# Kernel tuning notes

Hardware: AMD Instinct MI355X
Metric: run time of the kernel (lower is better)

The kernel has to match this reference:

```python
import jax, jax.numpy as jnp
import numpy as np

B, S, DIN, DOUT = 4, 2048, 4096, 4096
QMAX = 127  # 2**(8-1) - 1


def setup_inputs() -> dict:
    key = jax.random.key(0)
    k_x, k_w, k_b, k_ws = jax.random.split(key, 4)
    x = jax.random.normal(k_x, (B, S, DIN), dtype=jnp.float32)
    # int8-valued weights stored as int32 (as in the torch module's .int() weight)
    weight = jax.random.randint(k_w, (DOUT, DIN), -QMAX, QMAX + 1, dtype=jnp.int32)
    bias = jax.random.randint(k_b, (DOUT,), -10, 11, dtype=jnp.int32)
    # per-input-channel weight scale, shape (out_features, 1)
    weight_scale = (jax.random.uniform(k_ws, (DOUT, 1), dtype=jnp.float32) * 0.01 + 1e-4)
    input_scale = jnp.float32(0.02)
    output_scale = jnp.float32(0.05)
    return {
        "x": x,
        "weight": weight,
        "bias": bias,
        "weight_scale": weight_scale,
        "input_scale": input_scale,
        "output_scale": output_scale,
    }


def reference(x, weight, bias, weight_scale, input_scale, output_scale):
    # fake-quantize activations: round to int grid, then dequantize back to float
    xq = jnp.round(x / input_scale).astype(jnp.int32).astype(jnp.float32) * input_scale
    # dequantize weights: (O, I)
    w = weight.astype(jnp.float32) * weight_scale
    # fp32 GEMM: [B,S,I] x [I,O] -> [B,S,O]
    ret = jnp.einsum("bsi,oi->bso", xq, w)
    ret = ret + bias.astype(jnp.float32)
    # requantize output to int grid (int32 output, as in torch .int())
    return jnp.round(ret / output_scale).astype(jnp.int32)
```

## Files before the change

kernel.cpp:

```cpp
#include <hip/hip_runtime.h>
#include <stdint.h>

#define MDIM 8192
#define KDIM 4096
#define NDIM 4096
#define BK   64
#define NKT  (KDIM / BK)

typedef float f32x4 __attribute__((ext_vector_type(4)));
typedef __bf16 bf16x8 __attribute__((ext_vector_type(8)));
typedef short short8 __attribute__((ext_vector_type(8)));
typedef float fl4 __attribute__((ext_vector_type(4)));
typedef int i32x4 __attribute__((ext_vector_type(4)));

__device__ __forceinline__ short f2bf_bits(float f) {
    unsigned int u = __float_as_uint(f);
    u += 0x7fffu + ((u >> 16) & 1u);
    return (short)(u >> 16);
}

__device__ __forceinline__ void gload_lds16(const void* g, void* l) {
    __builtin_amdgcn_global_load_lds(
        (__attribute__((address_space(1))) void*)(uintptr_t)g,
        (__attribute__((address_space(3))) void*)(uintptr_t)l,
        16, 0, 0);
}

__global__ void __launch_bounds__(256) quant_x_kernel(const float* __restrict__ x,
                                                      short* __restrict__ xq,
                                                      const float* __restrict__ p_is) {
    const float inv_is = 1.0f / p_is[0];
    const int64_t stride = (int64_t)gridDim.x * 256 * 8;
    for (int64_t i = ((int64_t)blockIdx.x * 256 + threadIdx.x) * 8;
         i < (int64_t)MDIM * KDIM; i += stride) {
        fl4 a = __builtin_nontemporal_load((const fl4*)(x + i));
        fl4 b = __builtin_nontemporal_load((const fl4*)(x + i + 4));
        short8 o;
        o[0] = f2bf_bits(rintf(a[0] * inv_is));
        o[1] = f2bf_bits(rintf(a[1] * inv_is));
        o[2] = f2bf_bits(rintf(a[2] * inv_is));
        o[3] = f2bf_bits(rintf(a[3] * inv_is));
        o[4] = f2bf_bits(rintf(b[0] * inv_is));
        o[5] = f2bf_bits(rintf(b[1] * inv_is));
        o[6] = f2bf_bits(rintf(b[2] * inv_is));
        o[7] = f2bf_bits(rintf(b[3] * inv_is));
        *(short8*)(xq + i) = o;
    }
}

__global__ void __launch_bounds__(256) quant_w_kernel(const int* __restrict__ w,
                                                      short* __restrict__ wq) {
    const int64_t stride = (int64_t)gridDim.x * 256 * 8;
    for (int64_t i = ((int64_t)blockIdx.x * 256 + threadIdx.x) * 8;
         i < (int64_t)NDIM * KDIM; i += stride) {
        i32x4 a = __builtin_nontemporal_load((const i32x4*)(w + i));
        i32x4 b = __builtin_nontemporal_load((const i32x4*)(w + i + 4));
        short8 o;
        o[0] = f2bf_bits((float)a[0]);
        o[1] = f2bf_bits((float)a[1]);
        o[2] = f2bf_bits((float)a[2]);
        o[3] = f2bf_bits((float)a[3]);
        o[4] = f2bf_bits((float)b[0]);
        o[5] = f2bf_bits((float)b[1]);
        o[6] = f2bf_bits((float)b[2]);
        o[7] = f2bf_bits((float)b[3]);
        *(short8*)(wq + i) = o;
    }
}


#define PH_MID() do { \
    __builtin_amdgcn_s_barrier(); \
    asm volatile("s_waitcnt lgkmcnt(0)" ::: "memory"); \
    __builtin_amdgcn_sched_barrier(0); \
    __builtin_amdgcn_s_setprio(1); \
  } while (0)

#define PH_END() do { \
    __builtin_amdgcn_s_setprio(0); \
    __builtin_amdgcn_s_barrier(); \
    __builtin_amdgcn_sched_barrier(0); \
  } while (0)

#define PH_END_VM() do { \
    __builtin_amdgcn_s_setprio(0); \
    asm volatile("s_waitcnt vmcnt(4)" ::: "memory"); \
    __builtin_amdgcn_s_barrier(); \
    __builtin_amdgcn_sched_barrier(0); \
  } while (0)

__global__ void __launch_bounds__(512, 2) gemm_bf16_kernel(
    const short* __restrict__ A,
    const short* __restrict__ Bw,
    const int* __restrict__ bias,
    const float* __restrict__ wscale,
    const float* __restrict__ p_is,
    const float* __restrict__ p_os,
    int* __restrict__ out) {
    __shared__ __align__(16) short lds[65536];

    const int tid  = threadIdx.x;
    const int lane = tid & 63;
    const int wave = tid >> 6;
    const int quad = lane >> 4;
    const int r16  = lane & 15;
    const int sw   = r16 & 7;

    const int n0 = blockIdx.x * 256;
    const int m0 = blockIdx.y * 256;

    const int wmi = wave >> 2;
    const int wni = wave & 3;

    const int srow = tid >> 3;
    const int skc  = (tid & 7) ^ (srow & 7);
    const short* gA = A  + (int64_t)(m0 + srow) * KDIM + skc * 8;
    const short* gB = Bw + (int64_t)(n0 + srow) * KDIM + skc * 8;

#define STAGE_A(b, ha, T) do { \
    const short* _g = gA + (int64_t)((ha) * 128) * KDIM + (T) * BK; \
    gload_lds16(_g,             &lds[(b)*16384 + (ha)*8192 + wave*512]); \
    gload_lds16(_g + 64*KDIM,   &lds[(b)*16384 + (ha)*8192 + 4096 + wave*512]); \
  } while (0)
#define STAGE_B(b, ha, T) do { \
    const short* _g = gB + (int64_t)((ha) * 128) * KDIM + (T) * BK; \
    gload_lds16(_g,             &lds[32768 + (b)*16384 + (ha)*8192 + wave*512]); \
    gload_lds16(_g + 64*KDIM,   &lds[32768 + (b)*16384 + (ha)*8192 + 4096 + wave*512]); \
  } while (0)

    const int aRowOff = (wmi * 128 + r16) * 64;
    const int bRowOff = 32768 + (wni * 64 + r16) * 64;
    const int cOff0   = (quad ^ sw) * 8;
    const int cOff1   = cOff0 ^ 32;

#define LDA(b, mh, mi, ks) \
    (*(const bf16x8*)&lds[(b)*16384 + aRowOff + ((mh)*64 + (mi)*16)*64 + ((ks) ? cOff1 : cOff0)])
#define LDB(b, nh, nj, ks) \
    (*(const bf16x8*)&lds[(b)*16384 + bRowOff + ((nh)*32 + (nj)*16)*64 + ((ks) ? cOff1 : cOff0)])

#define READ_A(b, mh) do { \
    _Pragma("unroll") for (int mi = 0; mi < 4; ++mi) { \
        aR[mi][0] = LDA(b, mh, mi, 0); aR[mi][1] = LDA(b, mh, mi, 1); } \
  } while (0)
#define READ_B(b, nh, dst) do { \
    _Pragma("unroll") for (int nj = 0; nj < 2; ++nj) { \
        dst[nj][0] = LDB(b, nh, nj, 0); dst[nj][1] = LDB(b, nh, nj, 1); } \
  } while (0)
#define MFMA_Q(mh, nh, bsrc) do { \
    _Pragma("unroll") for (int mi = 0; mi < 4; ++mi) \
    _Pragma("unroll") for (int nj = 0; nj < 2; ++nj) \
    _Pragma("unroll") for (int ks = 0; ks < 2; ++ks) \
        acc[(mh)*4 + mi][(nh)*2 + nj] = __builtin_amdgcn_mfma_f32_16x16x32_bf16( \
            aR[mi][ks], bsrc[nj][ks], acc[(mh)*4 + mi][(nh)*2 + nj], 0, 0, 0); \
  } while (0)

    f32x4 acc[8][4];
#pragma unroll
    for (int i = 0; i < 8; ++i)
#pragma unroll
        for (int j = 0; j < 4; ++j) acc[i][j] = (f32x4)0.0f;

    bf16x8 aR[4][2], bLo[2][2], bHi[2][2];

    STAGE_A(0, 0, 0); STAGE_A(0, 1, 0);
    STAGE_B(0, 0, 0); STAGE_B(0, 1, 0);
    STAGE_B(1, 0, 1); STAGE_B(1, 1, 1);
    asm volatile("s_waitcnt vmcnt(4)" ::: "memory");
    __builtin_amdgcn_s_barrier();
    __builtin_amdgcn_sched_barrier(0);

    for (int it = 0; it < NKT / 2; ++it) {
        const int t1 = 2 * it + 1;
        const int tA = (2 * it + 2) & (NKT - 1);
        const int tB = (2 * it + 3) & (NKT - 1);

        READ_A(0, 0); READ_B(0, 0, bLo);
        STAGE_A(1, 0, t1);
        asm volatile("s_waitcnt lgkmcnt(8)" ::: "memory");
        PH_MID(); MFMA_Q(0, 0, bLo); PH_END();
        READ_B(0, 1, bHi);
        STAGE_A(1, 1, t1);
        PH_MID(); MFMA_Q(0, 1, bHi); PH_END();
        READ_A(0, 1);
        STAGE_B(0, 0, tA);
        PH_MID(); MFMA_Q(1, 1, bHi); PH_END();
        STAGE_B(0, 1, tA);
        PH_MID(); MFMA_Q(1, 0, bLo); PH_END_VM();
        READ_A(1, 0); READ_B(1, 0, bLo);
        STAGE_A(0, 0, tA);
        asm volatile("s_waitcnt lgkmcnt(8)" ::: "memory");
        PH_MID(); MFMA_Q(0, 0, bLo); PH_END();
        READ_B(1, 1, bHi);
        STAGE_A(0, 1, tA);
        PH_MID(); MFMA_Q(0, 1, bHi); PH_END();
        READ_A(1, 1);
        STAGE_B(1, 0, tB);
        PH_MID(); MFMA_Q(1, 1, bHi); PH_END();
        STAGE_B(1, 1, tB);
        PH_MID(); MFMA_Q(1, 0, bLo); PH_END_VM();
    }

    const float is = p_is[0];
    const float inv_os = 1.0f / p_os[0];
    const int colBase = n0 + wni * 64;

    float alpha[4], beta[4];
#pragma unroll
    for (int nj = 0; nj < 4; ++nj) {
        const int col = colBase + nj * 16 + r16;
        alpha[nj] = is * wscale[col] * inv_os;
        beta[nj]  = (float)bias[col] * inv_os;
    }

#pragma unroll
    for (int mi = 0; mi < 8; ++mi) {
        const int row0 = m0 + wmi * 128 + mi * 16 + quad * 4;
#pragma unroll
        for (int nj = 0; nj < 4; ++nj) {
            const int col = colBase + nj * 16 + r16;
#pragma unroll
            for (int reg = 0; reg < 4; ++reg) {
                const float v = acc[mi][nj][reg] * alpha[nj] + beta[nj];
                __builtin_nontemporal_store(__float2int_rn(v),
                                            out + (int64_t)(row0 + reg) * NDIM + col);
            }
        }
    }
}

extern "C" void kernel_launch(void* const* d_in, const int* in_sizes, int n_in,
                              void* d_out, int out_size, void* d_ws, size_t ws_size,
                              hipStream_t stream) {
    (void)in_sizes; (void)n_in; (void)out_size; (void)ws_size;
    const float* x      = (const float*)d_in[0];
    const int*   weight = (const int*)d_in[1];
    const int*   bias   = (const int*)d_in[2];
    const float* wscale = (const float*)d_in[3];
    const float* p_is   = (const float*)d_in[4];
    const float* p_os   = (const float*)d_in[5];

    short* xq = (short*)d_ws;
    short* wq = xq + (size_t)MDIM * KDIM;

    quant_x_kernel<<<2048, 256, 0, stream>>>(x, xq, p_is);
    quant_w_kernel<<<2048, 256, 0, stream>>>(weight, wq);

    dim3 grid(NDIM / 256, MDIM / 256);
    gemm_bf16_kernel<<<grid, 512, 0, stream>>>(xq, wq, bias, wscale, p_is, p_os, (int*)d_out);
}
```

Baseline: 468.3 us.

## Switch GEMM to fp16 MFMA, fuse quant kernels, swizzle workgroup mapping

```diff
diff --git a/kernel.cpp b/kernel.cpp
--- a/kernel.cpp
+++ b/kernel.cpp
@@ -8,16 +8,10 @@
 #define NKT  (KDIM / BK)
 
 typedef float f32x4 __attribute__((ext_vector_type(4)));
-typedef __bf16 bf16x8 __attribute__((ext_vector_type(8)));
+typedef _Float16 h16x8 __attribute__((ext_vector_type(8)));
 typedef short short8 __attribute__((ext_vector_type(8)));
 typedef float fl4 __attribute__((ext_vector_type(4)));
 typedef int i32x4 __attribute__((ext_vector_type(4)));
-
-__device__ __forceinline__ short f2bf_bits(float f) {
-    unsigned int u = __float_as_uint(f);
-    u += 0x7fffu + ((u >> 16) & 1u);
-    return (short)(u >> 16);
-}
 
 __device__ __forceinline__ void gload_lds16(const void* g, void* l) {
     __builtin_amdgcn_global_load_lds(
@@ -26,45 +20,46 @@
         16, 0, 0);
 }
 
-__global__ void __launch_bounds__(256) quant_x_kernel(const float* __restrict__ x,
-                                                      short* __restrict__ xq,
-                                                      const float* __restrict__ p_is) {
-    const float inv_is = 1.0f / p_is[0];
-    const int64_t stride = (int64_t)gridDim.x * 256 * 8;
-    for (int64_t i = ((int64_t)blockIdx.x * 256 + threadIdx.x) * 8;
-         i < (int64_t)MDIM * KDIM; i += stride) {
-        fl4 a = __builtin_nontemporal_load((const fl4*)(x + i));
-        fl4 b = __builtin_nontemporal_load((const fl4*)(x + i + 4));
-        short8 o;
-        o[0] = f2bf_bits(rintf(a[0] * inv_is));
-        o[1] = f2bf_bits(rintf(a[1] * inv_is));
-        o[2] = f2bf_bits(rintf(a[2] * inv_is));
-        o[3] = f2bf_bits(rintf(a[3] * inv_is));
-        o[4] = f2bf_bits(rintf(b[0] * inv_is));
-        o[5] = f2bf_bits(rintf(b[1] * inv_is));
-        o[6] = f2bf_bits(rintf(b[2] * inv_is));
-        o[7] = f2bf_bits(rintf(b[3] * inv_is));
-        *(short8*)(xq + i) = o;
-    }
-}
-
-__global__ void __launch_bounds__(256) quant_w_kernel(const int* __restrict__ w,
-                                                      short* __restrict__ wq) {
-    const int64_t stride = (int64_t)gridDim.x * 256 * 8;
-    for (int64_t i = ((int64_t)blockIdx.x * 256 + threadIdx.x) * 8;
-         i < (int64_t)NDIM * KDIM; i += stride) {
-        i32x4 a = __builtin_nontemporal_load((const i32x4*)(w + i));
-        i32x4 b = __builtin_nontemporal_load((const i32x4*)(w + i + 4));
-        short8 o;
-        o[0] = f2bf_bits((float)a[0]);
-        o[1] = f2bf_bits((float)a[1]);
-        o[2] = f2bf_bits((float)a[2]);
-        o[3] = f2bf_bits((float)a[3]);
-        o[4] = f2bf_bits((float)b[0]);
-        o[5] = f2bf_bits((float)b[1]);
-        o[6] = f2bf_bits((float)b[2]);
-        o[7] = f2bf_bits((float)b[3]);
-        *(short8*)(wq + i) = o;
+__global__ void __launch_bounds__(256) quant_kernel(const float* __restrict__ x,
+                                                    short* __restrict__ xq,
+                                                    const int* __restrict__ w,
+                                                    short* __restrict__ wq,
+                                                    const float* __restrict__ p_is) {
+    if (blockIdx.x < 2048) {
+        const float inv_is = 1.0f / p_is[0];
+        const int64_t stride = (int64_t)2048 * 256 * 8;
+        for (int64_t i = ((int64_t)blockIdx.x * 256 + threadIdx.x) * 8;
+             i < (int64_t)MDIM * KDIM; i += stride) {
+            fl4 a = __builtin_nontemporal_load((const fl4*)(x + i));
+            fl4 b = __builtin_nontemporal_load((const fl4*)(x + i + 4));
+            h16x8 o;
+            o[0] = (_Float16)rintf(a[0] * inv_is);
+            o[1] = (_Float16)rintf(a[1] * inv_is);
+            o[2] = (_Float16)rintf(a[2] * inv_is);
+            o[3] = (_Float16)rintf(a[3] * inv_is);
+            o[4] = (_Float16)rintf(b[0] * inv_is);
+            o[5] = (_Float16)rintf(b[1] * inv_is);
+            o[6] = (_Float16)rintf(b[2] * inv_is);
+            o[7] = (_Float16)rintf(b[3] * inv_is);
+            *(h16x8*)(xq + i) = o;
+        }
+    } else {
+        const int64_t stride = (int64_t)1024 * 256 * 8;
+        for (int64_t i = (((int64_t)blockIdx.x - 2048) * 256 + threadIdx.x) * 8;
+             i < (int64_t)NDIM * KDIM; i += stride) {
+            i32x4 a = *(const i32x4*)(w + i);
+            i32x4 b = *(const i32x4*)(w + i + 4);
+            h16x8 o;
+            o[0] = (_Float16)(float)a[0];
+            o[1] = (_Float16)(float)a[1];
+            o[2] = (_Float16)(float)a[2];
+            o[3] = (_Float16)(float)a[3];
+            o[4] = (_Float16)(float)b[0];
+            o[5] = (_Float16)(float)b[1];
+            o[6] = (_Float16)(float)b[2];
+            o[7] = (_Float16)(float)b[3];
+            *(h16x8*)(wq + i) = o;
+        }
     }
 }
 
@@ -89,7 +84,7 @@
     __builtin_amdgcn_sched_barrier(0); \
   } while (0)
 
-__global__ void __launch_bounds__(512, 2) gemm_bf16_kernel(
+__global__ void __launch_bounds__(512, 2) gemm_f16_kernel(
     const short* __restrict__ A,
     const short* __restrict__ Bw,
     const int* __restrict__ bias,
@@ -106,8 +101,12 @@
     const int r16  = lane & 15;
     const int sw   = r16 & 7;
 
-    const int n0 = blockIdx.x * 256;
-    const int m0 = blockIdx.y * 256;
+    const int flat  = blockIdx.y * gridDim.x + blockIdx.x;
+    const int wgid  = (flat & 7) * 64 + (flat >> 3);
+    const int m_blk = wgid >> 4;
+    const int n_blk = wgid & 15;
+    const int m0 = m_blk * 256;
+    const int n0 = n_blk * 256;
 
     const int wmi = wave >> 2;
     const int wni = wave & 3;
@@ -134,9 +133,9 @@
     const int cOff1   = cOff0 ^ 32;
 
 #define LDA(b, mh, mi, ks) \
-    (*(const bf16x8*)&lds[(b)*16384 + aRowOff + ((mh)*64 + (mi)*16)*64 + ((ks) ? cOff1 : cOff0)])
+    (*(const h16x8*)&lds[(b)*16384 + aRowOff + ((mh)*64 + (mi)*16)*64 + ((ks) ? cOff1 : cOff0)])
 #define LDB(b, nh, nj, ks) \
-    (*(const bf16x8*)&lds[(b)*16384 + bRowOff + ((nh)*32 + (nj)*16)*64 + ((ks) ? cOff1 : cOff0)])
+    (*(const h16x8*)&lds[(b)*16384 + bRowOff + ((nh)*32 + (nj)*16)*64 + ((ks) ? cOff1 : cOff0)])
 
 #define READ_A(b, mh) do { \
     _Pragma("unroll") for (int mi = 0; mi < 4; ++mi) { \
@@ -150,7 +149,7 @@
     _Pragma("unroll") for (int mi = 0; mi < 4; ++mi) \
     _Pragma("unroll") for (int nj = 0; nj < 2; ++nj) \
     _Pragma("unroll") for (int ks = 0; ks < 2; ++ks) \
-        acc[(mh)*4 + mi][(nh)*2 + nj] = __builtin_amdgcn_mfma_f32_16x16x32_bf16( \
+        acc[(mh)*4 + mi][(nh)*2 + nj] = __builtin_amdgcn_mfma_f32_16x16x32_f16( \
             aR[mi][ks], bsrc[nj][ks], acc[(mh)*4 + mi][(nh)*2 + nj], 0, 0, 0); \
   } while (0)
 
@@ -160,7 +159,7 @@
 #pragma unroll
         for (int j = 0; j < 4; ++j) acc[i][j] = (f32x4)0.0f;
 
-    bf16x8 aR[4][2], bLo[2][2], bHi[2][2];
+    h16x8 aR[4][2], bLo[2][2], bHi[2][2];
 
     STAGE_A(0, 0, 0); STAGE_A(0, 1, 0);
     STAGE_B(0, 0, 0); STAGE_B(0, 1, 0);
@@ -242,9 +241,8 @@
     short* xq = (short*)d_ws;
     short* wq = xq + (size_t)MDIM * KDIM;
 
-    quant_x_kernel<<<2048, 256, 0, stream>>>(x, xq, p_is);
-    quant_w_kernel<<<2048, 256, 0, stream>>>(weight, wq);
+    quant_kernel<<<3072, 256, 0, stream>>>(x, xq, weight, wq, p_is);
 
     dim3 grid(NDIM / 256, MDIM / 256);
-    gemm_bf16_kernel<<<grid, 512, 0, stream>>>(xq, wq, bias, wscale, p_is, p_os, (int*)d_out);
-}
+    gemm_f16_kernel<<<grid, 512, 0, stream>>>(xq, wq, bias, wscale, p_is, p_os, (int*)d_out);
+}
```

Result: no change. 474.8 us (+1.4%).
